# Kernel tuning notes

Measured on AMD Instinct MI355X. Metric: run time of the kernel, lower is better.

Reference implementation:

```python
import jax, jax.numpy as jnp
import numpy as np

N = 8192        # number of nodes (dense adjacency)
IN_DIM = 128    # GCN in_dim
OUT_DIM = 128   # GCN out_dim
MASK_THRESH = 0.8
NEG_INF = 1e9


def setup_inputs() -> dict:
    key = jax.random.key(0)
    kA, kX, kW = jax.random.split(key, 3)
    A = jax.random.uniform(kA, (N, N), dtype=jnp.float32)
    X = jax.random.normal(kX, (N, IN_DIM), dtype=jnp.float32)
    # nn.Linear(in_dim, out_dim): weight [out_dim, in_dim], bias [out_dim]
    W = jax.random.normal(kW, (OUT_DIM, IN_DIM), dtype=jnp.float32) * (1.0 / np.sqrt(IN_DIM))
    b = jnp.zeros((OUT_DIM,), dtype=jnp.float32)
    return {"A": A, "X": X, "W": W, "b": b}


def reference(A, X, W, b):
    # GCN.forward: A_norm = softmax(A - 1e9 * (A <= 0.8), axis=-1)
    # out = leaky_relu(A_norm @ Linear(X))   (relu=True path)
    logits = A - NEG_INF * (A <= MASK_THRESH).astype(A.dtype)   # [N, N]
    A_norm = jax.nn.softmax(logits, axis=-1)                     # row-wise softmax
    XW = X @ W.T + b                                             # [N, OUT_DIM]
    return jax.nn.leaky_relu(A_norm @ XW, negative_slope=0.01)   # [N, OUT_DIM]
```

## Files before the change

kernel.cpp:

```cpp
#include <hip/hip_runtime.h>
#include <hip/hip_bf16.h>

#define N_NODES 8192
#define DIM 128
#define MASK_THRESH 0.8f
#define RB 256
#define KSTEP 128

using f32x4  = __attribute__((ext_vector_type(4))) float;
using bf16x8 = __attribute__((ext_vector_type(8))) short;

static __device__ __forceinline__ short f2bf(float f) {
    unsigned u = __builtin_bit_cast(unsigned, f);
    u += 0x7fffu + ((u >> 16) & 1u);
    return (short)(u >> 16);
}

static __device__ __forceinline__ void gload16(const void* gsrc, void* ldst) {
    __builtin_amdgcn_global_load_lds(
        (const __attribute__((address_space(1))) unsigned int*)gsrc,
        (__attribute__((address_space(3))) unsigned int*)ldst,
        16, 0, 0);
}

__global__ __launch_bounds__(256) void build_vt_kernel(
    const float* __restrict__ X, const float* __restrict__ W,
    const float* __restrict__ bias, short* __restrict__ Vt) {
    __shared__ float xs[32][128];
    const int jt = blockIdx.x * 32;
    for (int e = threadIdx.x; e < 32 * 128; e += 256) {
        xs[e >> 7][e & 127] = X[(size_t)(jt + (e >> 7)) * DIM + (e & 127)];
    }
    __syncthreads();
    const int d  = threadIdx.x & 127;
    const int jh = threadIdx.x >> 7;
    float bv = bias[d];
    float acc[16];
#pragma unroll
    for (int i = 0; i < 16; i++) acc[i] = bv;
    const float* wrow = W + (size_t)d * DIM;
    for (int k = 0; k < DIM; k += 4) {
        f32x4 wv = *(const f32x4*)(wrow + k);
#pragma unroll
        for (int i = 0; i < 16; i++) {
            f32x4 xv = *(const f32x4*)(&xs[jh * 16 + i][k]);
            acc[i] += xv[0] * wv[0] + xv[1] * wv[1] + xv[2] * wv[2] + xv[3] * wv[3];
        }
    }
    bf16x8 o0, o1;
#pragma unroll
    for (int i = 0; i < 8; i++) { o0[i] = f2bf(acc[i]); o1[i] = f2bf(acc[8 + i]); }
    short* dst = Vt + (size_t)d * N_NODES + jt + jh * 16;
    *(bf16x8*)(dst)     = o0;
    *(bf16x8*)(dst + 8) = o1;
}

template <int WRITE_PARTIAL>
__global__ __launch_bounds__(512, 4) void fused_kernel(
    const float* __restrict__ A, const short* __restrict__ Vt,
    float* __restrict__ dst, float* __restrict__ Zp, int kchunk) {

    __shared__ __align__(16) char smem[49152];
    __shared__ float zs[8][16];

    short* vt_s = (short*)smem;
    float* a_s  = (float*)(smem + 32768);

    const int tid   = threadIdx.x;
    const int wid   = tid >> 6;
    const int lane  = tid & 63;
    const int row_a = lane & 15;
    const int kg    = lane >> 4;
    const int rgw   = wid >> 2;
    const int ksub  = wid & 3;

    const int rb     = blockIdx.x & (RB - 1);
    const int chunk  = blockIdx.x >> 8;
    const int r0     = rb * 32;
    const int k0     = chunk * kchunk;
    const int nsteps = kchunk >> 7;

    const short* vsrc[4]; short* vdst[4];
#pragma unroll
    for (int i = 0; i < 4; i++) {
        const int vrow = wid * 16 + i * 4 + (lane >> 4);
        vsrc[i] = Vt + (size_t)vrow * N_NODES + k0 + (size_t)(((lane & 15) ^ (vrow & 7)) * 8);
        vdst[i] = vt_s + (wid * 16 + i * 4) * KSTEP;
    }
    const float* asrc[2]; float* adst[2];
#pragma unroll
    for (int j = 0; j < 2; j++) {
        const int arow = wid * 4 + j * 2 + (lane >> 5);
        asrc[j] = A + (size_t)(r0 + arow) * N_NODES + k0 + (size_t)(((lane & 31) ^ (arow & 7)) * 4);
        adst[j] = a_s + (wid * 4 + j * 2) * KSTEP;
    }

    const int a_row  = rgw * 16 + row_a;
    const int a_off0 = a_row * KSTEP + ((ksub * 32 + kg * 8 + 0) ^ ((a_row & 7) * 4));
    const int a_off1 = a_row * KSTEP + ((ksub * 32 + kg * 8 + 4) ^ ((a_row & 7) * 4));
    int v_off[8];
#pragma unroll
    for (int t = 0; t < 8; t++) {
        const int d = t * 16 + row_a;
        v_off[t] = d * KSTEP + ((ksub * 32 + kg * 8) ^ ((d & 7) * 8));
    }

    f32x4 acc[8];
#pragma unroll
    for (int t = 0; t < 8; t++) acc[t] = (f32x4)0.0f;
    float zacc = 0.0f;

    for (int ks = 0; ks < nsteps; ks++) {
        __syncthreads();
#pragma unroll
        for (int i = 0; i < 4; i++) gload16(vsrc[i] + (size_t)ks * KSTEP, vdst[i]);
#pragma unroll
        for (int j = 0; j < 2; j++) gload16(asrc[j] + (size_t)ks * KSTEP, adst[j]);
        __syncthreads();

        const f32x4 av0 = *(const f32x4*)(a_s + a_off0);
        const f32x4 av1 = *(const f32x4*)(a_s + a_off1);
        float p[8];
#pragma unroll
        for (int i = 0; i < 4; i++) {
            p[i]     = (av0[i] > MASK_THRESH) ? __expf(av0[i]) : 0.0f;
            p[i + 4] = (av1[i] > MASK_THRESH) ? __expf(av1[i]) : 0.0f;
        }
        bf16x8 af;
#pragma unroll
        for (int i = 0; i < 8; i++) { zacc += p[i]; af[i] = f2bf(p[i]); }
#pragma unroll
        for (int t = 0; t < 8; t++) {
            const bf16x8 bv = *(const bf16x8*)(vt_s + v_off[t]);
            acc[t] = __builtin_amdgcn_mfma_f32_16x16x32_bf16(af, bv, acc[t], 0, 0, 0);
        }
    }

    zacc += __shfl_xor(zacc, 16);
    zacc += __shfl_xor(zacc, 32);
    __syncthreads();
    if (lane < 16) zs[wid][lane] = zacc;

    float* accs = (float*)smem;
#pragma unroll
    for (int rg = 0; rg < 2; rg++) {
        if (rgw == rg) {
#pragma unroll
            for (int t = 0; t < 8; t++)
#pragma unroll
                for (int r = 0; r < 4; r++)
                    accs[(ksub * 16 + kg * 4 + r) * 132 + t * 16 + row_a] = acc[t][r];
        }
        __syncthreads();
        {
            const int row = tid >> 5;
            const int c4  = (tid & 31) * 4;
            float s0 = 0, s1 = 0, s2 = 0, s3 = 0, zt = 0;
#pragma unroll
            for (int w = 0; w < 4; w++) {
                const float* p = &accs[(w * 16 + row) * 132 + c4];
                s0 += p[0]; s1 += p[1]; s2 += p[2]; s3 += p[3];
                zt += zs[rg * 4 + w][row];
            }
            const int orow = r0 + rg * 16 + row;
            if (WRITE_PARTIAL) {
                f32x4 v = {s0, s1, s2, s3};
                *(f32x4*)(dst + ((size_t)chunk * N_NODES + orow) * DIM + c4) = v;
            } else {
                f32x4 v;
                v[0] = s0 / zt; v[1] = s1 / zt; v[2] = s2 / zt; v[3] = s3 / zt;
#pragma unroll
                for (int j = 0; j < 4; j++) v[j] = (v[j] > 0.0f) ? v[j] : 0.01f * v[j];
                *(f32x4*)(dst + (size_t)orow * DIM + c4) = v;
            }
        }
        __syncthreads();
    }
    if (WRITE_PARTIAL && tid < 32) {
        const int rg = tid >> 4, ra = tid & 15;
        float z = 0.0f;
#pragma unroll
        for (int w = 0; w < 4; w++) z += zs[rg * 4 + w][ra];
        Zp[(size_t)chunk * N_NODES + r0 + rg * 16 + ra] = z;
    }
}

__global__ __launch_bounds__(256) void reduce_kernel(
    const float* __restrict__ num, const float* __restrict__ Zp,
    float* __restrict__ out, int S) {
    const size_t i4 = (size_t)blockIdx.x * 256 + threadIdx.x;
    const int r  = (int)(i4 >> 5);
    const int c4 = (int)(i4 & 31) * 4;
    f32x4 s = (f32x4)0.0f;
    float z = 0.0f;
    for (int p = 0; p < S; p++) {
        const f32x4 v = *(const f32x4*)(num + ((size_t)p * N_NODES + r) * DIM + c4);
        s += v;
        z += Zp[(size_t)p * N_NODES + r];
    }
    f32x4 o;
#pragma unroll
    for (int j = 0; j < 4; j++) {
        const float v = s[j] / z;
        o[j] = (v > 0.0f) ? v : 0.01f * v;
    }
    *(f32x4*)(out + (size_t)r * DIM + c4) = o;
}

extern "C" void kernel_launch(void* const* d_in, const int* in_sizes, int n_in,
                              void* d_out, int out_size, void* d_ws, size_t ws_size,
                              hipStream_t stream) {
    const float* A = (const float*)d_in[0];
    const float* X = (const float*)d_in[1];
    const float* W = (const float*)d_in[2];
    const float* b = (const float*)d_in[3];
    float* out = (float*)d_out;

    const size_t VT_BYTES = (size_t)DIM * N_NODES * 2;
    short* Vt = (short*)d_ws;
    build_vt_kernel<<<N_NODES / 32, 256, 0, stream>>>(X, W, b, Vt);

    const size_t per_split = ((size_t)N_NODES * DIM + N_NODES) * sizeof(float);
    int S = 1;
    for (int cand = 4; cand >= 1; cand >>= 1) {
        if (VT_BYTES + (size_t)cand * per_split <= ws_size) { S = cand; break; }
    }

    if (S >= 2) {
        float* num = (float*)((char*)d_ws + VT_BYTES);
        float* Zp  = num + (size_t)S * N_NODES * DIM;
        fused_kernel<1><<<RB * S, 512, 0, stream>>>(A, Vt, num, Zp, N_NODES / S);
        reduce_kernel<<<(N_NODES * DIM / 4) / 256, 256, 0, stream>>>(num, Zp, out, S);
    } else {
        fused_kernel<0><<<RB, 512, 0, stream>>>(A, Vt, out, nullptr, N_NODES);
    }
}
```

Baseline: 102.9 us.

## Store XW in MFMA fragment layout, read directly from global, double-buffer A

The XW projection is now written in a pre-swizzled fragment layout, so each lane loads its MFMA B operand straight from global memory (L2-resident) instead of staging Vt through LDS. Blocks shrink to 256 threads covering 16 rows with twice as many blocks, and A tiles are double-buffered in LDS with a prefetch of the next step, leaving one barrier per iteration. The aim is to cut LDS traffic and barriers in the memory-bound A stream. In exchange every block rereads the B fragments from global/L2, and there are more blocks in total.

```diff
diff --git a/kernel.cpp b/kernel.cpp
--- a/kernel.cpp
+++ b/kernel.cpp
@@ -4,7 +4,7 @@
 #define N_NODES 8192
 #define DIM 128
 #define MASK_THRESH 0.8f
-#define RB 256
+#define RB 512
 #define KSTEP 128
 
 using f32x4  = __attribute__((ext_vector_type(4))) float;
@@ -23,9 +23,9 @@
         16, 0, 0);
 }
 
-__global__ __launch_bounds__(256) void build_vt_kernel(
+__global__ __launch_bounds__(256) void build_vf_kernel(
     const float* __restrict__ X, const float* __restrict__ W,
-    const float* __restrict__ bias, short* __restrict__ Vt) {
+    const float* __restrict__ bias, short* __restrict__ Vf) {
     __shared__ float xs[32][128];
     const int jt = blockIdx.x * 32;
     for (int e = threadIdx.x; e < 32 * 128; e += 256) {
@@ -44,82 +44,71 @@
 #pragma unroll
         for (int i = 0; i < 16; i++) {
             f32x4 xv = *(const f32x4*)(&xs[jh * 16 + i][k]);
-            acc[i] += xv[0] * wv[0] + xv[1] * wv[1] + xv[2] * wv[2] + xv[3] * wv[3];
+            acc[i] = fmaf(xv[0], wv[0], acc[i]);
+            acc[i] = fmaf(xv[1], wv[1], acc[i]);
+            acc[i] = fmaf(xv[2], wv[2], acc[i]);
+            acc[i] = fmaf(xv[3], wv[3], acc[i]);
         }
     }
     bf16x8 o0, o1;
 #pragma unroll
     for (int i = 0; i < 8; i++) { o0[i] = f2bf(acc[i]); o1[i] = f2bf(acc[8 + i]); }
-    short* dst = Vt + (size_t)d * N_NODES + jt + jh * 16;
-    *(bf16x8*)(dst)     = o0;
-    *(bf16x8*)(dst + 8) = o1;
+    const int kb = jt >> 5;
+    const int t  = d >> 4;
+    short* base = Vf + ((size_t)(kb * 8 + t) * 64 + (d & 15) + 32 * jh) * 8;
+    *(bf16x8*)(base)       = o0;
+    *(bf16x8*)(base + 128) = o1;
 }
 
 template <int WRITE_PARTIAL>
-__global__ __launch_bounds__(512, 4) void fused_kernel(
-    const float* __restrict__ A, const short* __restrict__ Vt,
+__global__ __launch_bounds__(256, 4) void fused_kernel(
+    const float* __restrict__ A, const short* __restrict__ Vf,
     float* __restrict__ dst, float* __restrict__ Zp, int kchunk) {
 
-    __shared__ __align__(16) char smem[49152];
-    __shared__ float zs[8][16];
-
-    short* vt_s = (short*)smem;
-    float* a_s  = (float*)(smem + 32768);
+    __shared__ __align__(16) float smem[8448];
+    __shared__ float zs[4][16];
 
     const int tid   = threadIdx.x;
-    const int wid   = tid >> 6;
+    const int w     = tid >> 6;
     const int lane  = tid & 63;
     const int row_a = lane & 15;
     const int kg    = lane >> 4;
-    const int rgw   = wid >> 2;
-    const int ksub  = wid & 3;
-
-    const int rb     = blockIdx.x & (RB - 1);
-    const int chunk  = blockIdx.x >> 8;
-    const int r0     = rb * 32;
-    const int k0     = chunk * kchunk;
+    const int rb    = blockIdx.x & (RB - 1);
+    const int chunk = blockIdx.x >> 9;
+    const int r0    = rb * 16;
+    const int k0    = chunk * kchunk;
     const int nsteps = kchunk >> 7;
 
-    const short* vsrc[4]; short* vdst[4];
-#pragma unroll
-    for (int i = 0; i < 4; i++) {
-        const int vrow = wid * 16 + i * 4 + (lane >> 4);
-        vsrc[i] = Vt + (size_t)vrow * N_NODES + k0 + (size_t)(((lane & 15) ^ (vrow & 7)) * 8);
-        vdst[i] = vt_s + (wid * 16 + i * 4) * KSTEP;
-    }
-    const float* asrc[2]; float* adst[2];
-#pragma unroll
-    for (int j = 0; j < 2; j++) {
-        const int arow = wid * 4 + j * 2 + (lane >> 5);
-        asrc[j] = A + (size_t)(r0 + arow) * N_NODES + k0 + (size_t)(((lane & 31) ^ (arow & 7)) * 4);
-        adst[j] = a_s + (wid * 4 + j * 2) * KSTEP;
-    }
-
-    const int a_row  = rgw * 16 + row_a;
-    const int a_off0 = a_row * KSTEP + ((ksub * 32 + kg * 8 + 0) ^ ((a_row & 7) * 4));
-    const int a_off1 = a_row * KSTEP + ((ksub * 32 + kg * 8 + 4) ^ ((a_row & 7) * 4));
-    int v_off[8];
-#pragma unroll
-    for (int t = 0; t < 8; t++) {
-        const int d = t * 16 + row_a;
-        v_off[t] = d * KSTEP + ((ksub * 32 + kg * 8) ^ ((d & 7) * 8));
-    }
+    const float* asrc[2]; int adst_off[2];
+#pragma unroll
+    for (int i = 0; i < 2; i++) {
+        const int arow = w * 4 + i * 2 + (lane >> 5);
+        asrc[i] = A + (size_t)(r0 + arow) * N_NODES + k0 + (((lane & 31) ^ (arow & 7)) << 2);
+        adst_off[i] = (w * 4 + i * 2) * 128;
+    }
+    const int aoff0 = row_a * 128 + (((w * 8 + kg * 2 + 0) ^ (row_a & 7)) << 2);
+    const int aoff1 = row_a * 128 + (((w * 8 + kg * 2 + 1) ^ (row_a & 7)) << 2);
+    const short* vfp = Vf + ((size_t)((k0 >> 5) + w) * 8 * 64 + lane) * 8;
 
     f32x4 acc[8];
 #pragma unroll
     for (int t = 0; t < 8; t++) acc[t] = (f32x4)0.0f;
     float zacc = 0.0f;
 
+#pragma unroll
+    for (int i = 0; i < 2; i++) gload16(asrc[i], smem + adst_off[i]);
+
     for (int ks = 0; ks < nsteps; ks++) {
         __syncthreads();
-#pragma unroll
-        for (int i = 0; i < 4; i++) gload16(vsrc[i] + (size_t)ks * KSTEP, vdst[i]);
-#pragma unroll
-        for (int j = 0; j < 2; j++) gload16(asrc[j] + (size_t)ks * KSTEP, adst[j]);
-        __syncthreads();
-
-        const f32x4 av0 = *(const f32x4*)(a_s + a_off0);
-        const f32x4 av1 = *(const f32x4*)(a_s + a_off1);
+        if (ks + 1 < nsteps) {
+            float* nbuf = smem + ((ks + 1) & 1) * 2048;
+#pragma unroll
+            for (int i = 0; i < 2; i++)
+                gload16(asrc[i] + (size_t)(ks + 1) * KSTEP, nbuf + adst_off[i]);
+        }
+        const float* ab = smem + (ks & 1) * 2048;
+        const f32x4 av0 = *(const f32x4*)(ab + aoff0);
+        const f32x4 av1 = *(const f32x4*)(ab + aoff1);
         float p[8];
 #pragma unroll
         for (int i = 0; i < 4; i++) {
@@ -129,59 +118,56 @@
         bf16x8 af;
 #pragma unroll
         for (int i = 0; i < 8; i++) { zacc += p[i]; af[i] = f2bf(p[i]); }
+        const short* vstep = vfp + (size_t)ks * 16384;
 #pragma unroll
         for (int t = 0; t < 8; t++) {
-            const bf16x8 bv = *(const bf16x8*)(vt_s + v_off[t]);
+            const bf16x8 bv = *(const bf16x8*)(vstep + t * 512);
             acc[t] = __builtin_amdgcn_mfma_f32_16x16x32_bf16(af, bv, acc[t], 0, 0, 0);
         }
     }
 
     zacc += __shfl_xor(zacc, 16);
     zacc += __shfl_xor(zacc, 32);
+    if (lane < 16) zs[w][lane] = zacc;
+
     __syncthreads();
-    if (lane < 16) zs[wid][lane] = zacc;
-
-    float* accs = (float*)smem;
-#pragma unroll
-    for (int rg = 0; rg < 2; rg++) {
-        if (rgw == rg) {
-#pragma unroll
-            for (int t = 0; t < 8; t++)
-#pragma unroll
-                for (int r = 0; r < 4; r++)
-                    accs[(ksub * 16 + kg * 4 + r) * 132 + t * 16 + row_a] = acc[t][r];
-        }
-        __syncthreads();
-        {
-            const int row = tid >> 5;
-            const int c4  = (tid & 31) * 4;
-            float s0 = 0, s1 = 0, s2 = 0, s3 = 0, zt = 0;
-#pragma unroll
-            for (int w = 0; w < 4; w++) {
-                const float* p = &accs[(w * 16 + row) * 132 + c4];
-                s0 += p[0]; s1 += p[1]; s2 += p[2]; s3 += p[3];
-                zt += zs[rg * 4 + w][row];
+    float* accs = smem;
+#pragma unroll
+    for (int t = 0; t < 8; t++)
+#pragma unroll
+        for (int r = 0; r < 4; r++)
+            accs[(w * 16 + kg * 4 + r) * 132 + t * 16 + row_a] = acc[t][r];
+    __syncthreads();
+
+    {
+        const int row = tid >> 4;
+        const int c8  = (tid & 15) * 8;
+        float zt = zs[0][row] + zs[1][row] + zs[2][row] + zs[3][row];
+        f32x4 s0 = (f32x4)0.0f, s1 = (f32x4)0.0f;
+#pragma unroll
+        for (int ww = 0; ww < 4; ww++) {
+            const float* pp = &accs[(ww * 16 + row) * 132 + c8];
+            s0 += *(const f32x4*)(pp);
+            s1 += *(const f32x4*)(pp + 4);
+        }
+        if (WRITE_PARTIAL) {
+            float* nd = dst + ((size_t)chunk * N_NODES + r0 + row) * DIM + c8;
+            *(f32x4*)(nd)     = s0;
+            *(f32x4*)(nd + 4) = s1;
+            if (tid < 16) Zp[(size_t)chunk * N_NODES + r0 + tid] =
+                zs[0][tid] + zs[1][tid] + zs[2][tid] + zs[3][tid];
+        } else {
+            f32x4 o0, o1;
+#pragma unroll
+            for (int j = 0; j < 4; j++) {
+                float v0 = s0[j] / zt, v1 = s1[j] / zt;
+                o0[j] = (v0 > 0.0f) ? v0 : 0.01f * v0;
+                o1[j] = (v1 > 0.0f) ? v1 : 0.01f * v1;
             }
-            const int orow = r0 + rg * 16 + row;
-            if (WRITE_PARTIAL) {
-                f32x4 v = {s0, s1, s2, s3};
-                *(f32x4*)(dst + ((size_t)chunk * N_NODES + orow) * DIM + c4) = v;
-            } else {
-                f32x4 v;
-                v[0] = s0 / zt; v[1] = s1 / zt; v[2] = s2 / zt; v[3] = s3 / zt;
-#pragma unroll
-                for (int j = 0; j < 4; j++) v[j] = (v[j] > 0.0f) ? v[j] : 0.01f * v[j];
-                *(f32x4*)(dst + (size_t)orow * DIM + c4) = v;
-            }
-        }
-        __syncthreads();
-    }
-    if (WRITE_PARTIAL && tid < 32) {
-        const int rg = tid >> 4, ra = tid & 15;
-        float z = 0.0f;
-#pragma unroll
-        for (int w = 0; w < 4; w++) z += zs[rg * 4 + w][ra];
-        Zp[(size_t)chunk * N_NODES + r0 + rg * 16 + ra] = z;
+            float* od = dst + (size_t)(r0 + row) * DIM + c8;
+            *(f32x4*)(od)     = o0;
+            *(f32x4*)(od + 4) = o1;
+        }
     }
 }
 
@@ -194,8 +180,7 @@
     f32x4 s = (f32x4)0.0f;
     float z = 0.0f;
     for (int p = 0; p < S; p++) {
-        const f32x4 v = *(const f32x4*)(num + ((size_t)p * N_NODES + r) * DIM + c4);
-        s += v;
+        s += *(const f32x4*)(num + ((size_t)p * N_NODES + r) * DIM + c4);
         z += Zp[(size_t)p * N_NODES + r];
     }
     f32x4 o;
@@ -216,22 +201,22 @@
     const float* b = (const float*)d_in[3];
     float* out = (float*)d_out;
 
-    const size_t VT_BYTES = (size_t)DIM * N_NODES * 2;
-    short* Vt = (short*)d_ws;
-    build_vt_kernel<<<N_NODES / 32, 256, 0, stream>>>(X, W, b, Vt);
+    const size_t VF_BYTES = (size_t)DIM * N_NODES * 2;
+    short* Vf = (short*)d_ws;
+    build_vf_kernel<<<N_NODES / 32, 256, 0, stream>>>(X, W, b, Vf);
 
     const size_t per_split = ((size_t)N_NODES * DIM + N_NODES) * sizeof(float);
     int S = 1;
     for (int cand = 4; cand >= 1; cand >>= 1) {
-        if (VT_BYTES + (size_t)cand * per_split <= ws_size) { S = cand; break; }
+        if (VF_BYTES + (size_t)cand * per_split <= ws_size) { S = cand; break; }
     }
 
     if (S >= 2) {
-        float* num = (float*)((char*)d_ws + VT_BYTES);
+        float* num = (float*)((char*)d_ws + VF_BYTES);
         float* Zp  = num + (size_t)S * N_NODES * DIM;
-        fused_kernel<1><<<RB * S, 512, 0, stream>>>(A, Vt, num, Zp, N_NODES / S);
+        fused_kernel<1><<<RB * S, 256, 0, stream>>>(A, Vf, num, Zp, N_NODES / S);
         reduce_kernel<<<(N_NODES * DIM / 4) / 256, 256, 0, stream>>>(num, Zp, out, S);
     } else {
-        fused_kernel<0><<<RB, 512, 0, stream>>>(A, Vt, out, nullptr, N_NODES);
-    }
-}
+        fused_kernel<0><<<RB, 256, 0, stream>>>(A, Vf, out, nullptr, N_NODES);
+    }
+}
```

Result: slower. 125.1 us (+21.6%).
